# Kernel optimization log

Hardware: AMD Instinct MI355X
Metric: run time of the kernel (lower is better)

Reference implementation:

```python
import jax, jax.numpy as jnp
import numpy as np

NEG_MASK_SCALE = -1e-09  # faithful to source (source uses -1e-09, likely intended -1e9)


def setup_inputs() -> dict:
    key0 = jax.random.key(0)
    ks = jax.random.split(key0, 7)
    B, Q, K, H = 4, 256, 1024, 128
    return {
        "query": jax.random.normal(ks[0], (B, Q, H), dtype=jnp.float32),
        "key": jax.random.normal(ks[1], (B, K, H), dtype=jnp.float32),
        "value": jax.random.normal(ks[2], (B, K, H), dtype=jnp.float32),
        "mask": jax.random.randint(ks[3], (B, Q, K), 0, 2).astype(jnp.int32),
        "Wq": jax.random.normal(ks[4], (H, H), dtype=jnp.float32) * (1.0 / np.sqrt(H)),
        "Wk": jax.random.normal(ks[5], (H, H), dtype=jnp.float32) * (1.0 / np.sqrt(H)),
        "v": jax.random.normal(ks[6], (H,), dtype=jnp.float32) * (1.0 / np.sqrt(H)),
    }


def reference(query, key, value, mask, Wq, Wk, v):
    # Projections: torch Linear computes x @ W.T
    q_proj = jnp.einsum("bqd,hd->bqh", query, Wq)  # (B, Q, H)
    k_proj = jnp.einsum("bkd,hd->bkh", key, Wk)    # (B, K, H)
    # Additive (Bahdanau) score: v . tanh(q_proj[:, :, None] + k_proj[:, None])
    feat = jnp.tanh(q_proj[:, :, None, :] + k_proj[:, None, :, :])  # (B, Q, K, H)
    score = jnp.einsum("bqkh,h->bqk", feat, v)                      # (B, Q, K)
    score = score + NEG_MASK_SCALE * (1.0 - mask.astype(score.dtype))
    attention_weights = jax.nn.softmax(score, axis=-1)              # (B, Q, K)
    context_vector = jnp.einsum("bqk,bkv->bqv", attention_weights, value)  # (B, Q, V)
    return attention_weights, context_vector
```

## Files before the change

kernel.cpp:

```cpp
#include <hip/hip_runtime.h>

#define Bb 4
#define Qn 256
#define Kn 1024
#define Hn 128

constexpr float SCALE = 2.88539008177792681f;

#if __has_builtin(__builtin_amdgcn_exp2f)
#define EXP2F(x) __builtin_amdgcn_exp2f(x)
#else
#define EXP2F(x) exp2f(x)
#endif
#if __has_builtin(__builtin_amdgcn_rcpf)
#define RCPF(x) __builtin_amdgcn_rcpf(x)
#else
#define RCPF(x) (1.0f / (x))
#endif

__global__ __launch_bounds__(128) void proj_kernel(const float* __restrict__ query,
                                                   const float* __restrict__ key,
                                                   const float* __restrict__ Wq,
                                                   const float* __restrict__ Wk,
                                                   float* __restrict__ eq,
                                                   float* __restrict__ ekT) {
    __shared__ float4 xs[128];
    const int tid = threadIdx.x;
    const bool isQ = blockIdx.x < (Bb * Qn / 4);
    const int r0 = (isQ ? blockIdx.x : blockIdx.x - Bb * Qn / 4) * 4;
    const float* x = isQ ? query : key;
    const float* W = isQ ? Wq : Wk;

    xs[tid] = ((const float4*)(x + (size_t)r0 * Hn))[tid];
    __syncthreads();
    const float4* W4 = (const float4*)W + (size_t)tid * (Hn / 4);
    float acc0 = 0.f, acc1 = 0.f, acc2 = 0.f, acc3 = 0.f;
#pragma unroll 8
    for (int d = 0; d < Hn / 4; ++d) {
        float4 w = W4[d];
        float4 a0 = xs[d];
        float4 a1 = xs[32 + d];
        float4 a2 = xs[64 + d];
        float4 a3 = xs[96 + d];
        acc0 = fmaf(w.x, a0.x, fmaf(w.y, a0.y, fmaf(w.z, a0.z, fmaf(w.w, a0.w, acc0))));
        acc1 = fmaf(w.x, a1.x, fmaf(w.y, a1.y, fmaf(w.z, a1.z, fmaf(w.w, a1.w, acc1))));
        acc2 = fmaf(w.x, a2.x, fmaf(w.y, a2.y, fmaf(w.z, a2.z, fmaf(w.w, a2.w, acc2))));
        acc3 = fmaf(w.x, a3.x, fmaf(w.y, a3.y, fmaf(w.z, a3.z, fmaf(w.w, a3.w, acc3))));
    }
    if (isQ) {
        eq[(size_t)(r0 + 0) * Hn + tid] = EXP2F(acc0 * SCALE);
        eq[(size_t)(r0 + 1) * Hn + tid] = EXP2F(acc1 * SCALE);
        eq[(size_t)(r0 + 2) * Hn + tid] = EXP2F(acc2 * SCALE);
        eq[(size_t)(r0 + 3) * Hn + tid] = EXP2F(acc3 * SCALE);
    } else {
        const int b = r0 / Kn;
        const int k0 = r0 % Kn;
        float4 res = make_float4(EXP2F(acc0 * SCALE), EXP2F(acc1 * SCALE),
                                 EXP2F(acc2 * SCALE), EXP2F(acc3 * SCALE));
        ((float4*)ekT)[(size_t)(b * Hn + tid) * (Kn / 4) + (k0 >> 2)] = res;
    }
}

__global__ __launch_bounds__(1024) void fused_attn_kernel(const float* __restrict__ eq,
                                                          const float* __restrict__ ekT,
                                                          const float* __restrict__ v,
                                                          const float* __restrict__ value,
                                                          float* __restrict__ attn,
                                                          float* __restrict__ ctx) {
    const int tid = threadIdx.x;
    const int q0 = blockIdx.x * 2;
    const int b = blockIdx.y;

    __shared__ __align__(16) float2 qs[Hn][2];
    __shared__ __align__(16) float sc[2][Kn];
    __shared__ float red[32];
    __shared__ float pl[4][2][Hn];

    if (tid < Hn) {
        float e0 = eq[((size_t)b * Qn + q0) * Hn + tid];
        float e1 = eq[((size_t)b * Qn + q0 + 1) * Hn + tid];
        float vh = v[tid];
        qs[tid][0] = make_float2(e0, vh);
        qs[tid][1] = make_float2(e1, vh);
    }
    __syncthreads();

    const int qq = tid >> 9;
    const int t = tid & 511;
    const float2* kp2 = (const float2*)(ekT + (size_t)b * Hn * Kn) + t;
    float a0 = 0.f, a1 = 0.f;
#pragma unroll 8
    for (int h = 0; h < Hn; ++h) {
        float2 kv = kp2[(size_t)h * (Kn / 2)];
        float2 qv = qs[h][qq];
        float r;
        r = RCPF(fmaf(qv.x, kv.x, 1.0f)); a0 = fmaf(qv.y, r, a0);
        r = RCPF(fmaf(qv.x, kv.y, 1.0f)); a1 = fmaf(qv.y, r, a1);
    }

    const int lane = tid & 63, wv = tid >> 6;
    float mn = fminf(a0, a1);
#pragma unroll
    for (int off = 32; off; off >>= 1) mn = fminf(mn, __shfl_xor(mn, off));
    if (lane == 0) red[wv] = mn;
    __syncthreads();
    {
        const float* rq = &red[qq * 8];
        mn = fminf(fminf(fminf(rq[0], rq[1]), fminf(rq[2], rq[3])),
                   fminf(fminf(rq[4], rq[5]), fminf(rq[6], rq[7])));
    }

    float e0 = EXP2F((mn - a0) * SCALE);
    float e1 = EXP2F((mn - a1) * SCALE);
    float s = e0 + e1;
#pragma unroll
    for (int off = 32; off; off >>= 1) s += __shfl_xor(s, off);
    if (lane == 0) red[16 + wv] = s;
    __syncthreads();
    {
        const float* rq = &red[16 + qq * 8];
        s = ((rq[0] + rq[1]) + (rq[2] + rq[3])) + ((rq[4] + rq[5]) + (rq[6] + rq[7]));
    }
    const float inv = RCPF(s);

    float2 w2 = make_float2(e0 * inv, e1 * inv);
    ((float2*)&sc[qq][0])[t] = w2;
    ((float2*)(attn + ((size_t)b * Qn + q0 + qq) * Kn))[t] = w2;
    __syncthreads();

    const int hq = tid & 127;
    const int q2 = (tid >> 7) & 1;
    const int kq = tid >> 8;
    const float* vb = value + ((size_t)b * Kn + kq * (Kn / 4)) * Hn + hq;
    const float4* wrow = (const float4*)&sc[q2][kq * (Kn / 4)];
    float acc = 0.f;
#pragma unroll 4
    for (int k4 = 0; k4 < Kn / 16; ++k4) {
        float4 wv4 = wrow[k4];
        acc = fmaf(wv4.x, vb[(size_t)(4 * k4 + 0) * Hn], acc);
        acc = fmaf(wv4.y, vb[(size_t)(4 * k4 + 1) * Hn], acc);
        acc = fmaf(wv4.z, vb[(size_t)(4 * k4 + 2) * Hn], acc);
        acc = fmaf(wv4.w, vb[(size_t)(4 * k4 + 3) * Hn], acc);
    }
    pl[kq][q2][hq] = acc;
    __syncthreads();
    if (tid < 256) {
        const int qo = tid >> 7, ho = tid & 127;
        ctx[((size_t)b * Qn + q0 + qo) * Hn + ho] =
            (pl[0][qo][ho] + pl[1][qo][ho]) + (pl[2][qo][ho] + pl[3][qo][ho]);
    }
}

extern "C" void kernel_launch(void* const* d_in, const int* in_sizes, int n_in,
                              void* d_out, int out_size, void* d_ws, size_t ws_size,
                              hipStream_t stream) {
    const float* query = (const float*)d_in[0];
    const float* key = (const float*)d_in[1];
    const float* value = (const float*)d_in[2];
    const float* Wq = (const float*)d_in[4];
    const float* Wk = (const float*)d_in[5];
    const float* v = (const float*)d_in[6];

    float* out = (float*)d_out;
    float* attn = out;
    float* ctx = out + (size_t)Bb * Qn * Kn;

    float* ws = (float*)d_ws;
    float* eq = ws;
    float* ekT = ws + 131072;

    proj_kernel<<<dim3(Bb * Qn / 4 + Bb * Kn / 4), dim3(128), 0, stream>>>(
        query, key, Wq, Wk, eq, ekT);
    fused_attn_kernel<<<dim3(Qn / 2, Bb), dim3(1024), 0, stream>>>(
        eq, ekT, v, value, attn, ctx);
}
```

Measured before the change: 129.1 us.

## Process four queries per block to reuse each key feature load

The fused attention kernel now handles four query rows per block instead of two. Each thread owns one key and computes four scores, so every ekT value loaded from global memory is reused across four queries. The context matmul is re-split into 8 key chunks with float4 value loads and a final 8-way partial reduction. This halves the number of blocks to 256 and raises per-thread register use, which may lower occupancy and parallelism.

```diff
diff --git a/kernel.cpp b/kernel.cpp
--- a/kernel.cpp
+++ b/kernel.cpp
@@ -4,6 +4,7 @@
 #define Qn 256
 #define Kn 1024
 #define Hn 128
+#define QT 4
 
 constexpr float SCALE = 2.88539008177792681f;
 
@@ -68,86 +69,116 @@
                                                           float* __restrict__ attn,
                                                           float* __restrict__ ctx) {
     const int tid = threadIdx.x;
-    const int q0 = blockIdx.x * 2;
+    const int q0 = blockIdx.x * QT;
     const int b = blockIdx.y;
 
-    __shared__ __align__(16) float2 qs[Hn][2];
-    __shared__ __align__(16) float sc[2][Kn];
-    __shared__ float red[32];
-    __shared__ float pl[4][2][Hn];
-
-    if (tid < Hn) {
-        float e0 = eq[((size_t)b * Qn + q0) * Hn + tid];
-        float e1 = eq[((size_t)b * Qn + q0 + 1) * Hn + tid];
-        float vh = v[tid];
-        qs[tid][0] = make_float2(e0, vh);
-        qs[tid][1] = make_float2(e1, vh);
-    }
-    __syncthreads();
-
-    const int qq = tid >> 9;
-    const int t = tid & 511;
-    const float2* kp2 = (const float2*)(ekT + (size_t)b * Hn * Kn) + t;
-    float a0 = 0.f, a1 = 0.f;
+    __shared__ __align__(16) float4 qs4[Hn];
+    __shared__ float vs[Hn];
+    __shared__ __align__(16) float sc[QT][Kn];
+    __shared__ float red[16][QT];
+    __shared__ __align__(16) float4 pl[8][QT][Hn / 4];
+
+    if (tid < Hn) vs[tid] = v[tid];
+    if (tid < QT * Hn) {
+        const int q = tid >> 7, h = tid & 127;
+        ((float*)&qs4[h])[q] = eq[((size_t)b * Qn + q0 + q) * Hn + h];
+    }
+    __syncthreads();
+
+    const int k = tid;
+    const float* ek = ekT + (size_t)b * Hn * Kn + k;
+    float a0 = 0.f, a1 = 0.f, a2 = 0.f, a3 = 0.f;
 #pragma unroll 8
     for (int h = 0; h < Hn; ++h) {
-        float2 kv = kp2[(size_t)h * (Kn / 2)];
-        float2 qv = qs[h][qq];
+        const float kv = ek[(size_t)h * Kn];
+        const float4 qv = qs4[h];
+        const float vh = vs[h];
         float r;
-        r = RCPF(fmaf(qv.x, kv.x, 1.0f)); a0 = fmaf(qv.y, r, a0);
-        r = RCPF(fmaf(qv.x, kv.y, 1.0f)); a1 = fmaf(qv.y, r, a1);
+        r = RCPF(fmaf(qv.x, kv, 1.0f)); a0 = fmaf(vh, r, a0);
+        r = RCPF(fmaf(qv.y, kv, 1.0f)); a1 = fmaf(vh, r, a1);
+        r = RCPF(fmaf(qv.z, kv, 1.0f)); a2 = fmaf(vh, r, a2);
+        r = RCPF(fmaf(qv.w, kv, 1.0f)); a3 = fmaf(vh, r, a3);
     }
 
     const int lane = tid & 63, wv = tid >> 6;
-    float mn = fminf(a0, a1);
-#pragma unroll
-    for (int off = 32; off; off >>= 1) mn = fminf(mn, __shfl_xor(mn, off));
-    if (lane == 0) red[wv] = mn;
-    __syncthreads();
-    {
-        const float* rq = &red[qq * 8];
-        mn = fminf(fminf(fminf(rq[0], rq[1]), fminf(rq[2], rq[3])),
-                   fminf(fminf(rq[4], rq[5]), fminf(rq[6], rq[7])));
-    }
-
-    float e0 = EXP2F((mn - a0) * SCALE);
-    float e1 = EXP2F((mn - a1) * SCALE);
-    float s = e0 + e1;
-#pragma unroll
-    for (int off = 32; off; off >>= 1) s += __shfl_xor(s, off);
-    if (lane == 0) red[16 + wv] = s;
-    __syncthreads();
-    {
-        const float* rq = &red[16 + qq * 8];
-        s = ((rq[0] + rq[1]) + (rq[2] + rq[3])) + ((rq[4] + rq[5]) + (rq[6] + rq[7]));
-    }
-    const float inv = RCPF(s);
-
-    float2 w2 = make_float2(e0 * inv, e1 * inv);
-    ((float2*)&sc[qq][0])[t] = w2;
-    ((float2*)(attn + ((size_t)b * Qn + q0 + qq) * Kn))[t] = w2;
-    __syncthreads();
-
-    const int hq = tid & 127;
-    const int q2 = (tid >> 7) & 1;
-    const int kq = tid >> 8;
-    const float* vb = value + ((size_t)b * Kn + kq * (Kn / 4)) * Hn + hq;
-    const float4* wrow = (const float4*)&sc[q2][kq * (Kn / 4)];
-    float acc = 0.f;
+    float m0 = a0, m1 = a1, m2 = a2, m3 = a3;
+#pragma unroll
+    for (int off = 32; off; off >>= 1) {
+        m0 = fminf(m0, __shfl_xor(m0, off));
+        m1 = fminf(m1, __shfl_xor(m1, off));
+        m2 = fminf(m2, __shfl_xor(m2, off));
+        m3 = fminf(m3, __shfl_xor(m3, off));
+    }
+    if (lane == 0) {
+        red[wv][0] = m0; red[wv][1] = m1; red[wv][2] = m2; red[wv][3] = m3;
+    }
+    __syncthreads();
+    m0 = red[0][0]; m1 = red[0][1]; m2 = red[0][2]; m3 = red[0][3];
+#pragma unroll
+    for (int w = 1; w < 16; ++w) {
+        m0 = fminf(m0, red[w][0]); m1 = fminf(m1, red[w][1]);
+        m2 = fminf(m2, red[w][2]); m3 = fminf(m3, red[w][3]);
+    }
+    __syncthreads();
+
+    float e0 = EXP2F((m0 - a0) * SCALE);
+    float e1 = EXP2F((m1 - a1) * SCALE);
+    float e2 = EXP2F((m2 - a2) * SCALE);
+    float e3 = EXP2F((m3 - a3) * SCALE);
+    float s0 = e0, s1 = e1, s2 = e2, s3 = e3;
+#pragma unroll
+    for (int off = 32; off; off >>= 1) {
+        s0 += __shfl_xor(s0, off);
+        s1 += __shfl_xor(s1, off);
+        s2 += __shfl_xor(s2, off);
+        s3 += __shfl_xor(s3, off);
+    }
+    if (lane == 0) {
+        red[wv][0] = s0; red[wv][1] = s1; red[wv][2] = s2; red[wv][3] = s3;
+    }
+    __syncthreads();
+    s0 = red[0][0]; s1 = red[0][1]; s2 = red[0][2]; s3 = red[0][3];
+#pragma unroll
+    for (int w = 1; w < 16; ++w) {
+        s0 += red[w][0]; s1 += red[w][1]; s2 += red[w][2]; s3 += red[w][3];
+    }
+
+    const float w0 = e0 * RCPF(s0);
+    const float w1 = e1 * RCPF(s1);
+    const float w2 = e2 * RCPF(s2);
+    const float w3 = e3 * RCPF(s3);
+    sc[0][k] = w0; sc[1][k] = w1; sc[2][k] = w2; sc[3][k] = w3;
+    float* arow = attn + ((size_t)b * Qn + q0) * Kn + k;
+    arow[0 * Kn] = w0; arow[1 * Kn] = w1; arow[2 * Kn] = w2; arow[3 * Kn] = w3;
+    __syncthreads();
+
+    const int kc = tid >> 7;
+    const int cq = (tid >> 5) & 3;
+    const int h4 = tid & 31;
+    const float4* vb = (const float4*)(value + ((size_t)b * Kn + kc * 128) * Hn) + h4;
+    const float* wr = &sc[cq][kc * 128];
+    float4 acc = make_float4(0.f, 0.f, 0.f, 0.f);
 #pragma unroll 4
-    for (int k4 = 0; k4 < Kn / 16; ++k4) {
-        float4 wv4 = wrow[k4];
-        acc = fmaf(wv4.x, vb[(size_t)(4 * k4 + 0) * Hn], acc);
-        acc = fmaf(wv4.y, vb[(size_t)(4 * k4 + 1) * Hn], acc);
-        acc = fmaf(wv4.z, vb[(size_t)(4 * k4 + 2) * Hn], acc);
-        acc = fmaf(wv4.w, vb[(size_t)(4 * k4 + 3) * Hn], acc);
-    }
-    pl[kq][q2][hq] = acc;
-    __syncthreads();
-    if (tid < 256) {
-        const int qo = tid >> 7, ho = tid & 127;
-        ctx[((size_t)b * Qn + q0 + qo) * Hn + ho] =
-            (pl[0][qo][ho] + pl[1][qo][ho]) + (pl[2][qo][ho] + pl[3][qo][ho]);
+    for (int kk = 0; kk < 128; ++kk) {
+        const float wgt = wr[kk];
+        const float4 vv = vb[(size_t)kk * (Hn / 4)];
+        acc.x = fmaf(wgt, vv.x, acc.x);
+        acc.y = fmaf(wgt, vv.y, acc.y);
+        acc.z = fmaf(wgt, vv.z, acc.z);
+        acc.w = fmaf(wgt, vv.w, acc.w);
+    }
+    pl[kc][cq][h4] = acc;
+    __syncthreads();
+    if (tid < QT * Hn / 4) {
+        const int q = tid >> 5, h = tid & 31;
+        float4 r0 = pl[0][q][h], r1 = pl[1][q][h], r2 = pl[2][q][h], r3 = pl[3][q][h];
+        float4 r4 = pl[4][q][h], r5 = pl[5][q][h], r6 = pl[6][q][h], r7 = pl[7][q][h];
+        float4 sum;
+        sum.x = ((r0.x + r1.x) + (r2.x + r3.x)) + ((r4.x + r5.x) + (r6.x + r7.x));
+        sum.y = ((r0.y + r1.y) + (r2.y + r3.y)) + ((r4.y + r5.y) + (r6.y + r7.y));
+        sum.z = ((r0.z + r1.z) + (r2.z + r3.z)) + ((r4.z + r5.z) + (r6.z + r7.z));
+        sum.w = ((r0.w + r1.w) + (r2.w + r3.w)) + ((r4.w + r5.w) + (r6.w + r7.w));
+        ((float4*)(ctx + ((size_t)b * Qn + q0 + q) * Hn))[h] = sum;
     }
 }
 
@@ -171,6 +202,6 @@
 
     proj_kernel<<<dim3(Bb * Qn / 4 + Bb * Kn / 4), dim3(128), 0, stream>>>(
         query, key, Wq, Wk, eq, ekT);
-    fused_attn_kernel<<<dim3(Qn / 2, Bb), dim3(1024), 0, stream>>>(
+    fused_attn_kernel<<<dim3(Qn / QT, Bb), dim3(1024), 0, stream>>>(
         eq, ekT, v, value, attn, ctx);
 }
```

New measurement: 117.7 us. 8.9% less time.
